# Kernel optimization log

Hardware: AMD Instinct MI355X
Metric: run time of the kernel (lower is better)

## Reference

```python
import jax, jax.numpy as jnp
import numpy as np

N = 50000
E = 800000
H = 128

def setup_inputs() -> dict:
    key = jax.random.key(0)
    ks = jax.random.split(key, 12)
    s = 1.0 / np.sqrt(H)
    inp = {
        "x": jax.random.normal(ks[0], (N, H), dtype=jnp.float32),
        "edge_index": jax.random.randint(ks[1], (2, E), 0, N, dtype=jnp.int64),
        "edge_attr": jax.random.normal(ks[2], (E, H), dtype=jnp.float32),
        # linear_edge: Linear(3H, H)
        "We": jax.random.uniform(ks[3], (3 * H, H), jnp.float32, -s, s),
        "be": jnp.zeros((H,), jnp.float32),
        # attention_layer.W: Linear(H, H)
        "Wg": jax.random.uniform(ks[4], (H, H), jnp.float32, -s, s),
        "bg": jnp.zeros((H,), jnp.float32),
        # attention_layer.a: Linear(2H, 1)
        "Wa": jax.random.uniform(ks[5], (2 * H, 1), jnp.float32, -s, s),
        "ba": jnp.zeros((1,), jnp.float32),
        # linear_out: Linear(H, H)
        "Wo": jax.random.uniform(ks[6], (H, H), jnp.float32, -s, s),
        "bo": jnp.zeros((H,), jnp.float32),
    }
    return inp


def reference(x, edge_index, edge_attr, We, be, Wg, bg, Wa, ba, Wo, bo):
    # PyG MessagePassing (flow=source_to_target): j = edge_index[0] (source),
    # i = edge_index[1] (target); aggregation scatters to edge_index[1].
    src = edge_index[0]
    dst = edge_index[1]

    # message: SiLU(Linear(cat[x_i, x_j, edge_attr]))  -- split We to avoid a [E,3H] concat
    m = jax.nn.silu(x[dst] @ We[:H] + x[src] @ We[H:2 * H] + edge_attr @ We[2 * H:] + be)  # [E,H]
    agg = jax.ops.segment_sum(m, dst, num_segments=N)  # [N,H] scatter-add aggregate

    # GraphAttentionLayer: row, col = edge_index -> row=edge_index[0], col=edge_index[1]
    h = agg @ Wg + bg  # [N,H]
    score = jax.nn.leaky_relu(h[src] @ Wa[:H] + h[dst] @ Wa[H:] + ba, negative_slope=0.2)  # [E,1]
    # softmax over the last dim of size 1 -> all ones (faithful to original); dropout off (eval)
    alpha = jax.nn.softmax(score, axis=-1)  # [E,1]
    attn_out = jax.ops.segment_sum(alpha * h[dst], src, num_segments=N)  # [N,H]

    return attn_out @ Wo + bo  # linear_out
```

## Files before the change

kernel.cpp:

```cpp
#include <hip/hip_runtime.h>

#define N_NODES 50000
#define N_EDGES 800000

typedef unsigned short u16;
typedef unsigned int u32;
typedef __attribute__((ext_vector_type(8))) short short8;
typedef __attribute__((ext_vector_type(4))) short s16x4;
typedef __attribute__((ext_vector_type(4))) float f32x4;

__device__ __forceinline__ u16 f2bf(float f) {
    union { float f; u32 u; } v; v.f = f;
    u32 r = v.u + 0x7FFFu + ((v.u >> 16) & 1u);
    return (u16)(r >> 16);
}

__device__ __forceinline__ float bf2f(u16 h) {
    union { u32 u; float f; } v; v.u = ((u32)h) << 16;
    return v.f;
}

__global__ __launch_bounds__(256) void compute_wc(const float* __restrict__ Wg,
                                                  const float* __restrict__ bg,
                                                  const float* __restrict__ Wo,
                                                  float* __restrict__ Wc,
                                                  float* __restrict__ bc) {
    int b = blockIdx.x;
    if (b < 8) {
        for (int i = 0; i < 8; ++i) {
            int o = b * 2048 + i * 256 + threadIdx.x;
            int k = o >> 7, n = o & 127;
            float s = 0.f;
            for (int j = 0; j < 128; ++j) s += Wg[k * 128 + j] * Wo[j * 128 + n];
            Wc[o] = s;
        }
    } else if (threadIdx.x < 128) {
        int n = threadIdx.x;
        float s = 0.f;
        for (int j = 0; j < 128; ++j) s += bg[j] * Wo[j * 128 + n];
        bc[n] = s;
    }
}

__global__ __launch_bounds__(256) void pack_all(const float* __restrict__ We,
                                                const float* __restrict__ Wc,
                                                const float* __restrict__ be,
                                                u16* __restrict__ PB1,
                                                u16* __restrict__ PB3,
                                                u16* __restrict__ PBc,
                                                float* __restrict__ b256) {
    int bid = blockIdx.x;
    int which = bid >> 3;
    const float* src;
    u16* dst;
    int tOff = 0;
    if (which == 0) { src = We; dst = PB1; }
    else if (which == 1) { src = We + 16384; dst = PB1; tOff = 8; }
    else if (which == 2) { src = We + 32768; dst = PB3; }
    else { src = Wc; dst = PBc; }
    int f = ((bid & 7) << 8) + threadIdx.x;
    int t = f >> 8, c = (f >> 6) & 3, lane = f & 63;
    int q = lane >> 4, n = lane & 15;
    const float* s = src + (size_t)(c * 32 + q * 8) * 128 + t * 16 + n;
    u16* dp = dst + ((((size_t)(t + tOff) * 4 + c) * 64 + lane) * 8);
#pragma unroll
    for (int j = 0; j < 8; ++j) dp[j] = f2bf(s[(size_t)j * 128]);
    if (bid == 0) b256[threadIdx.x] = (threadIdx.x < 128) ? be[threadIdx.x] : 0.f;
}

__global__ __launch_bounds__(256) void hist_kernel(const int* __restrict__ srcIdx,
                                                   const int* __restrict__ dstIdx,
                                                   int* __restrict__ degD,
                                                   int* __restrict__ degS) {
    int e = blockIdx.x * 256 + threadIdx.x;
    if (e >= N_EDGES) return;
    atomicAdd(&degD[dstIdx[e]], 1);
    atomicAdd(&degS[srcIdx[e]], 1);
}

__global__ __launch_bounds__(256) void scan_kernel(const int* __restrict__ degD,
                                                   const int* __restrict__ degS,
                                                   int* __restrict__ offD, int* __restrict__ curD,
                                                   int* __restrict__ offS, int* __restrict__ curS) {
    const int* deg = blockIdx.x ? degS : degD;
    int* off = blockIdx.x ? offS : offD;
    int* cur = blockIdx.x ? curS : curD;
    __shared__ int buf[256];
    const int CHUNK = 196;
    int tid = threadIdx.x;
    int s0 = tid * CHUNK, s1 = s0 + CHUNK;
    if (s1 > N_NODES) s1 = N_NODES;
    int s = 0;
    for (int i = s0; i < s1; ++i) s += deg[i];
    buf[tid] = s;
    __syncthreads();
    for (int o = 1; o < 256; o <<= 1) {
        int v = (tid >= o) ? buf[tid - o] : 0;
        __syncthreads();
        buf[tid] += v;
        __syncthreads();
    }
    int run = (tid > 0) ? buf[tid - 1] : 0;
    for (int i = s0; i < s1; ++i) {
        off[i] = run;
        cur[i] = run;
        run += deg[i];
    }
    if (tid == 255) off[N_NODES] = buf[255];
}

__global__ __launch_bounds__(256) void scatter_kernel(const int* __restrict__ srcIdx,
                                                      const int* __restrict__ dstIdx,
                                                      int* __restrict__ curD,
                                                      int* __restrict__ curS,
                                                      int* __restrict__ sd_ea,
                                                      int* __restrict__ sd_src,
                                                      int* __restrict__ ss_dst) {
    int e = blockIdx.x * 256 + threadIdx.x;
    if (e >= N_EDGES) return;
    int s = srcIdx[e], d = dstIdx[e];
    int p = atomicAdd(&curD[d], 1);
    sd_ea[p] = e;
    sd_src[p] = s;
    int p2 = atomicAdd(&curS[s], 1);
    ss_dst[p2] = d;
}

__global__ __launch_bounds__(256) void gemm_mfma(const void* __restrict__ Ap,
                                                 const u16* __restrict__ PB,
                                                 const float* __restrict__ bias,
                                                 const float* __restrict__ bias2,
                                                 const int* __restrict__ rowdeg,
                                                 void* __restrict__ outp,
                                                 int M, int Ctiles, int flags) {
    int tid = threadIdx.x;
    int wave = tid >> 6;
    int lane = tid & 63;
    int strip = blockIdx.x * 4 + wave;
    int row0 = strip * 16;
    if (row0 >= M) return;
    int q = lane >> 4, n = lane & 15;
    int C = Ctiles * 16;

    short8 a[4];
    if (flags & 2) {
        const u16* ap = (const u16*)Ap + (size_t)(row0 + n) * 128 + q * 8;
#pragma unroll
        for (int c = 0; c < 4; ++c) a[c] = *(const short8*)(ap + c * 32);
    } else {
        const float* ap = (const float*)Ap + (size_t)(row0 + n) * 128 + q * 8;
#pragma unroll
        for (int c = 0; c < 4; ++c) {
            f32x4 f0 = *(const f32x4*)(ap + c * 32);
            f32x4 f1 = *(const f32x4*)(ap + c * 32 + 4);
            short8 t;
#pragma unroll
            for (int j = 0; j < 4; ++j) {
                t[j] = (short)f2bf(f0[j]);
                t[4 + j] = (short)f2bf(f1[j]);
            }
            a[c] = t;
        }
    }

    float rb[4] = {0.f, 0.f, 0.f, 0.f};
    if (flags & 4) {
#pragma unroll
        for (int r = 0; r < 4; ++r) rb[r] = (float)rowdeg[row0 + q * 4 + r];
    }

    for (int t = 0; t < Ctiles; ++t) {
        f32x4 acc = {0.f, 0.f, 0.f, 0.f};
#pragma unroll
        for (int c = 0; c < 4; ++c) {
            short8 b = *(const short8*)(PB + (((size_t)t * 4 + c) * 64 + lane) * 8);
            acc = __builtin_amdgcn_mfma_f32_16x16x32_bf16(a[c], b, acc, 0, 0, 0);
        }
        int col = t * 16 + n;
        float bv = bias ? bias[col] : 0.f;
        float b2 = (flags & 4) ? bias2[col] : 0.f;
#pragma unroll
        for (int r = 0; r < 4; ++r) {
            int row = row0 + q * 4 + r;
            float v = acc[r] + bv + rb[r] * b2;
            if (flags & 1)
                ((u16*)outp)[(size_t)row * C + col] = f2bf(v);
            else
                ((float*)outp)[(size_t)row * C + col] = v;
        }
    }
}

__global__ __launch_bounds__(256) void agg_fused(const float* __restrict__ EA,
                                                 const u16* __restrict__ PB3,
                                                 const int* __restrict__ offD,
                                                 const int* __restrict__ sd_ea,
                                                 const int* __restrict__ sd_src,
                                                 const u16* __restrict__ T1,
                                                 u16* __restrict__ agg) {
    __shared__ u16 ldsT[4][16][132];
    int tid = threadIdx.x;
    int wave = tid >> 6;
    int lane = tid & 63;
    int node = blockIdx.x * 4 + wave;
    if (node >= N_NODES) return;
    int q = lane >> 4, n = lane & 15;
    int segS = offD[node], segE = offD[node + 1];

    float g1[8], rowAcc[8];
#pragma unroll
    for (int t = 0; t < 8; ++t) {
        g1[t] = bf2f(T1[(size_t)node * 256 + t * 16 + n]);
        rowAcc[t] = 0.f;
    }

    int rl = lane >> 2, cb = lane & 3;
    u16* myL = &ldsT[wave][0][0];

    for (int base = segS; base < segE; base += 16) {
        int er = base + n;
        if (er > segE - 1) er = segE - 1;
        const float* ap = EA + (size_t)sd_ea[er] * 128 + q * 8;
        short8 a[4];
#pragma unroll
        for (int c = 0; c < 4; ++c) {
            f32x4 f0 = *(const f32x4*)(ap + c * 32);
            f32x4 f1 = *(const f32x4*)(ap + c * 32 + 4);
            short8 t;
#pragma unroll
            for (int j = 0; j < 4; ++j) {
                t[j] = (short)f2bf(f0[j]);
                t[4 + j] = (short)f2bf(f1[j]);
            }
            a[c] = t;
        }

        int erL = base + rl;
        if (erL > segE - 1) erL = segE - 1;
        const u16* tb = T1 + (size_t)sd_src[erL] * 256 + 128;
        asm volatile("s_waitcnt lgkmcnt(0)" ::: "memory");
#pragma unroll
        for (int i = 0; i < 4; ++i) {
            short8 v = *(const short8*)(tb + (i * 4 + cb) * 8);
            s16x4 lo = __builtin_shufflevector(v, v, 0, 1, 2, 3);
            s16x4 hi = __builtin_shufflevector(v, v, 4, 5, 6, 7);
            *(s16x4*)(myL + rl * 132 + (i * 4 + cb) * 8) = lo;
            *(s16x4*)(myL + rl * 132 + (i * 4 + cb) * 8 + 4) = hi;
        }
        asm volatile("s_waitcnt lgkmcnt(0)" ::: "memory");

        bool val[4];
#pragma unroll
        for (int r = 0; r < 4; ++r) val[r] = (base + q * 4 + r) < segE;

#pragma unroll
        for (int t = 0; t < 8; ++t) {
            f32x4 acc = {0.f, 0.f, 0.f, 0.f};
#pragma unroll
            for (int c = 0; c < 4; ++c) {
                short8 b = *(const short8*)(PB3 + (((size_t)t * 4 + c) * 64 + lane) * 8);
                acc = __builtin_amdgcn_mfma_f32_16x16x32_bf16(a[c], b, acc, 0, 0, 0);
            }
#pragma unroll
            for (int r = 0; r < 4; ++r) {
                float v = acc[r] + g1[t] + bf2f(myL[(q * 4 + r) * 132 + t * 16 + n]);
                float m = v * __builtin_amdgcn_rcpf(1.f + __expf(-v));
                rowAcc[t] += val[r] ? m : 0.f;
            }
        }
    }
#pragma unroll
    for (int t = 0; t < 8; ++t) {
        float v = rowAcc[t];
        v += __shfl_xor(v, 16, 64);
        v += __shfl_xor(v, 32, 64);
        if (lane < 16) agg[(size_t)node * 128 + t * 16 + lane] = f2bf(v);
    }
}

__global__ __launch_bounds__(256) void attn_gather(const int* __restrict__ offS,
                                                   const int* __restrict__ ss_dst,
                                                   const u16* __restrict__ hsrc,
                                                   float* __restrict__ attn) {
    int tid = threadIdx.x;
    int wave = tid >> 6;
    int lane = tid & 63;
    int node = blockIdx.x * 4 + wave;
    if (node >= N_NODES) return;
    int e0 = offS[node], e1 = offS[node + 1];
    int half = lane >> 5;
    int l = lane & 31;
    float a0 = 0.f, a1 = 0.f, a2 = 0.f, a3 = 0.f;
    int e = e0 + half;
    for (; e + 6 < e1; e += 8) {
        int d0 = ss_dst[e], d1 = ss_dst[e + 2], d2 = ss_dst[e + 4], d3 = ss_dst[e + 6];
        uint2 h0 = *(const uint2*)(hsrc + (size_t)d0 * 128 + l * 4);
        uint2 h1 = *(const uint2*)(hsrc + (size_t)d1 * 128 + l * 4);
        uint2 h2 = *(const uint2*)(hsrc + (size_t)d2 * 128 + l * 4);
        uint2 h3 = *(const uint2*)(hsrc + (size_t)d3 * 128 + l * 4);
        a0 += bf2f((u16)(h0.x & 0xFFFFu)) + bf2f((u16)(h1.x & 0xFFFFu)) +
              bf2f((u16)(h2.x & 0xFFFFu)) + bf2f((u16)(h3.x & 0xFFFFu));
        a1 += bf2f((u16)(h0.x >> 16)) + bf2f((u16)(h1.x >> 16)) +
              bf2f((u16)(h2.x >> 16)) + bf2f((u16)(h3.x >> 16));
        a2 += bf2f((u16)(h0.y & 0xFFFFu)) + bf2f((u16)(h1.y & 0xFFFFu)) +
              bf2f((u16)(h2.y & 0xFFFFu)) + bf2f((u16)(h3.y & 0xFFFFu));
        a3 += bf2f((u16)(h0.y >> 16)) + bf2f((u16)(h1.y >> 16)) +
              bf2f((u16)(h2.y >> 16)) + bf2f((u16)(h3.y >> 16));
    }
    for (; e < e1; e += 2) {
        int d = ss_dst[e];
        uint2 hv = *(const uint2*)(hsrc + (size_t)d * 128 + l * 4);
        a0 += bf2f((u16)(hv.x & 0xFFFFu));
        a1 += bf2f((u16)(hv.x >> 16));
        a2 += bf2f((u16)(hv.y & 0xFFFFu));
        a3 += bf2f((u16)(hv.y >> 16));
    }
    a0 += __shfl_xor(a0, 32, 64);
    a1 += __shfl_xor(a1, 32, 64);
    a2 += __shfl_xor(a2, 32, 64);
    a3 += __shfl_xor(a3, 32, 64);
    if (half == 0) {
        f32x4 o;
        o[0] = a0; o[1] = a1; o[2] = a2; o[3] = a3;
        *(f32x4*)(attn + (size_t)node * 128 + l * 4) = o;
    }
}

extern "C" void kernel_launch(void* const* d_in, const int* in_sizes, int n_in,
                              void* d_out, int out_size, void* d_ws, size_t ws_size,
                              hipStream_t stream) {
    const float* x  = (const float*)d_in[0];
    const int* ei   = (const int*)d_in[1];
    const float* ea = (const float*)d_in[2];
    const float* We = (const float*)d_in[3];
    const float* be = (const float*)d_in[4];
    const float* Wg = (const float*)d_in[5];
    const float* bg = (const float*)d_in[6];
    const float* Wo = (const float*)d_in[9];
    const float* bo = (const float*)d_in[10];
    float* out = (float*)d_out;

    const int* srcIdx = ei;
    const int* dstIdx = ei + N_EDGES;

    char* ws = (char*)d_ws;
    u16*   PB1     = (u16*)(ws + 0);
    u16*   PB3     = (u16*)(ws + 65536);
    u16*   PBc     = (u16*)(ws + 98304);
    float* Wc      = (float*)(ws + 131072);
    float* bias256 = (float*)(ws + 196608);
    float* bc      = (float*)(ws + 197632);
    u16*   T1      = (u16*)(ws + 262144);
    float* attn    = (float*)(ws + 262144);
    u16*   agg     = (u16*)(ws + 25862144);
    int*   degD    = (int*)(ws + 51462144);
    int*   degS    = (int*)(ws + 51662144);
    int*   offD    = (int*)(ws + 51862144);
    int*   offS    = (int*)(ws + 52062160);
    int*   curD    = (int*)(ws + 52262176);
    int*   curS    = (int*)(ws + 52462176);
    int*   sd_ea   = (int*)(ws + 52662176);
    int*   sd_src  = (int*)(ws + 55862176);
    int*   ss_dst  = (int*)(ws + 59062176);

    hipMemsetAsync(degD, 0, 400000, stream);

    compute_wc<<<9, 256, 0, stream>>>(Wg, bg, Wo, Wc, bc);
    pack_all<<<32, 256, 0, stream>>>(We, Wc, be, PB1, PB3, PBc, bias256);

    hist_kernel<<<3125, 256, 0, stream>>>(srcIdx, dstIdx, degD, degS);
    scan_kernel<<<2, 256, 0, stream>>>(degD, degS, offD, curD, offS, curS);
    scatter_kernel<<<3125, 256, 0, stream>>>(srcIdx, dstIdx, curD, curS, sd_ea, sd_src, ss_dst);

    gemm_mfma<<<782, 256, 0, stream>>>(x, PB1, bias256, nullptr, nullptr, T1, N_NODES, 16, 1);

    agg_fused<<<12500, 256, 0, stream>>>(ea, PB3, offD, sd_ea, sd_src, T1, agg);

    attn_gather<<<12500, 256, 0, stream>>>(offS, ss_dst, agg, attn);

    gemm_mfma<<<782, 256, 0, stream>>>(attn, PBc, bo, bc, degS, out, N_NODES, 8, 4);

    (void)in_sizes; (void)n_in; (void)out_size; (void)ws_size;
}
```

Measured before the change: 1.102 ms.

## Fold source-node projection into edge MFMA and rebalance aggregation kernels

The edge kernel no longer gathers a precomputed x_src@We projection from T1 through LDS. It instead gathers bf16-cast x rows for the source node and runs a K=256 MFMA over the concatenated edge_attr and x_src against a combined packed weight. Each node's 128 output columns are now split across two waves, and edge id and source index are stored as one int2 to cut index loads. The attention gather now has a whole wave read 64 indices at once and broadcast them by shuffle, with each lane loading 2 bf16 values per edge. In exchange, the edge path does twice the MFMA work, and a separate cast kernel plus extra x-row gathers are added.

```diff
diff --git a/kernel.cpp b/kernel.cpp
--- a/kernel.cpp
+++ b/kernel.cpp
@@ -6,8 +6,8 @@
 typedef unsigned short u16;
 typedef unsigned int u32;
 typedef __attribute__((ext_vector_type(8))) short short8;
-typedef __attribute__((ext_vector_type(4))) short s16x4;
 typedef __attribute__((ext_vector_type(4))) float f32x4;
+typedef __attribute__((ext_vector_type(2))) float f32x2;
 
 __device__ __forceinline__ u16 f2bf(float f) {
     union { float f; u32 u; } v; v.f = f;
@@ -44,28 +44,35 @@
 
 __global__ __launch_bounds__(256) void pack_all(const float* __restrict__ We,
                                                 const float* __restrict__ Wc,
-                                                const float* __restrict__ be,
                                                 u16* __restrict__ PB1,
-                                                u16* __restrict__ PB3,
-                                                u16* __restrict__ PBc,
-                                                float* __restrict__ b256) {
+                                                u16* __restrict__ PBe,
+                                                u16* __restrict__ PBc) {
     int bid = blockIdx.x;
-    int which = bid >> 3;
-    const float* src;
-    u16* dst;
-    int tOff = 0;
-    if (which == 0) { src = We; dst = PB1; }
-    else if (which == 1) { src = We + 16384; dst = PB1; tOff = 8; }
-    else if (which == 2) { src = We + 32768; dst = PB3; }
-    else { src = Wc; dst = PBc; }
-    int f = ((bid & 7) << 8) + threadIdx.x;
-    int t = f >> 8, c = (f >> 6) & 3, lane = f & 63;
+    int job = bid >> 3;
+    int t = bid & 7;
+    const float* src; u16* dst; int slotBase, CH;
+    if (job == 0)      { src = We;         dst = PB1; slotBase = 0; CH = 4; }
+    else if (job == 1) { src = We + 32768; dst = PBe; slotBase = 0; CH = 8; }
+    else if (job == 2) { src = We + 16384; dst = PBe; slotBase = 4; CH = 8; }
+    else               { src = Wc;         dst = PBc; slotBase = 0; CH = 4; }
+    int c = threadIdx.x >> 6;
+    int lane = threadIdx.x & 63;
     int q = lane >> 4, n = lane & 15;
     const float* s = src + (size_t)(c * 32 + q * 8) * 128 + t * 16 + n;
-    u16* dp = dst + ((((size_t)(t + tOff) * 4 + c) * 64 + lane) * 8);
+    u16* dp = dst + (((size_t)(t * CH + slotBase + c) * 64 + lane) * 8);
 #pragma unroll
     for (int j = 0; j < 8; ++j) dp[j] = f2bf(s[(size_t)j * 128]);
-    if (bid == 0) b256[threadIdx.x] = (threadIdx.x < 128) ? be[threadIdx.x] : 0.f;
+}
+
+__global__ __launch_bounds__(256) void cast_bf16(const float* __restrict__ x,
+                                                 u16* __restrict__ X2) {
+    size_t i = (size_t)(blockIdx.x * 256 + threadIdx.x) * 8;
+    f32x4 v0 = *(const f32x4*)(x + i);
+    f32x4 v1 = *(const f32x4*)(x + i + 4);
+    short8 o;
+#pragma unroll
+    for (int j = 0; j < 4; ++j) { o[j] = (short)f2bf(v0[j]); o[4 + j] = (short)f2bf(v1[j]); }
+    *(short8*)(X2 + i) = o;
 }
 
 __global__ __launch_bounds__(256) void hist_kernel(const int* __restrict__ srcIdx,
@@ -113,15 +120,13 @@
                                                       const int* __restrict__ dstIdx,
                                                       int* __restrict__ curD,
                                                       int* __restrict__ curS,
-                                                      int* __restrict__ sd_ea,
-                                                      int* __restrict__ sd_src,
+                                                      int2* __restrict__ sdP,
                                                       int* __restrict__ ss_dst) {
     int e = blockIdx.x * 256 + threadIdx.x;
     if (e >= N_EDGES) return;
     int s = srcIdx[e], d = dstIdx[e];
     int p = atomicAdd(&curD[d], 1);
-    sd_ea[p] = e;
-    sd_src[p] = s;
+    sdP[p] = make_int2(e, s);
     int p2 = atomicAdd(&curS[s], 1);
     ss_dst[p2] = d;
 }
@@ -192,36 +197,36 @@
 }
 
 __global__ __launch_bounds__(256) void agg_fused(const float* __restrict__ EA,
-                                                 const u16* __restrict__ PB3,
+                                                 const u16* __restrict__ X2,
+                                                 const u16* __restrict__ PBe,
                                                  const int* __restrict__ offD,
-                                                 const int* __restrict__ sd_ea,
-                                                 const int* __restrict__ sd_src,
-                                                 const u16* __restrict__ T1,
+                                                 const int2* __restrict__ sdP,
+                                                 const u16* __restrict__ T1a,
                                                  u16* __restrict__ agg) {
-    __shared__ u16 ldsT[4][16][132];
     int tid = threadIdx.x;
     int wave = tid >> 6;
     int lane = tid & 63;
-    int node = blockIdx.x * 4 + wave;
+    int node = blockIdx.x * 2 + (wave >> 1);
     if (node >= N_NODES) return;
+    int cg = wave & 1;
     int q = lane >> 4, n = lane & 15;
     int segS = offD[node], segE = offD[node + 1];
-
-    float g1[8], rowAcc[8];
-#pragma unroll
-    for (int t = 0; t < 8; ++t) {
-        g1[t] = bf2f(T1[(size_t)node * 256 + t * 16 + n]);
+    const u16* pb = PBe + (size_t)cg * 16384;
+
+    float g1[4], rowAcc[4];
+#pragma unroll
+    for (int t = 0; t < 4; ++t) {
+        g1[t] = bf2f(T1a[(size_t)node * 128 + (cg * 4 + t) * 16 + n]);
         rowAcc[t] = 0.f;
     }
-
-    int rl = lane >> 2, cb = lane & 3;
-    u16* myL = &ldsT[wave][0][0];
 
     for (int base = segS; base < segE; base += 16) {
         int er = base + n;
         if (er > segE - 1) er = segE - 1;
-        const float* ap = EA + (size_t)sd_ea[er] * 128 + q * 8;
-        short8 a[4];
+        int2 es = sdP[er];
+        const float* ap = EA + (size_t)es.x * 128 + q * 8;
+        const u16* xp = X2 + (size_t)es.y * 128 + q * 8;
+        short8 a[8];
 #pragma unroll
         for (int c = 0; c < 4; ++c) {
             f32x4 f0 = *(const f32x4*)(ap + c * 32);
@@ -233,48 +238,34 @@
                 t[4 + j] = (short)f2bf(f1[j]);
             }
             a[c] = t;
-        }
-
-        int erL = base + rl;
-        if (erL > segE - 1) erL = segE - 1;
-        const u16* tb = T1 + (size_t)sd_src[erL] * 256 + 128;
-        asm volatile("s_waitcnt lgkmcnt(0)" ::: "memory");
-#pragma unroll
-        for (int i = 0; i < 4; ++i) {
-            short8 v = *(const short8*)(tb + (i * 4 + cb) * 8);
-            s16x4 lo = __builtin_shufflevector(v, v, 0, 1, 2, 3);
-            s16x4 hi = __builtin_shufflevector(v, v, 4, 5, 6, 7);
-            *(s16x4*)(myL + rl * 132 + (i * 4 + cb) * 8) = lo;
-            *(s16x4*)(myL + rl * 132 + (i * 4 + cb) * 8 + 4) = hi;
-        }
-        asm volatile("s_waitcnt lgkmcnt(0)" ::: "memory");
-
+            a[4 + c] = *(const short8*)(xp + c * 32);
+        }
         bool val[4];
 #pragma unroll
         for (int r = 0; r < 4; ++r) val[r] = (base + q * 4 + r) < segE;
 
 #pragma unroll
-        for (int t = 0; t < 8; ++t) {
+        for (int t = 0; t < 4; ++t) {
             f32x4 acc = {0.f, 0.f, 0.f, 0.f};
 #pragma unroll
-            for (int c = 0; c < 4; ++c) {
-                short8 b = *(const short8*)(PB3 + (((size_t)t * 4 + c) * 64 + lane) * 8);
+            for (int c = 0; c < 8; ++c) {
+                short8 b = *(const short8*)(pb + (((size_t)t * 8 + c) * 64 + lane) * 8);
                 acc = __builtin_amdgcn_mfma_f32_16x16x32_bf16(a[c], b, acc, 0, 0, 0);
             }
 #pragma unroll
             for (int r = 0; r < 4; ++r) {
-                float v = acc[r] + g1[t] + bf2f(myL[(q * 4 + r) * 132 + t * 16 + n]);
+                float v = acc[r] + g1[t];
                 float m = v * __builtin_amdgcn_rcpf(1.f + __expf(-v));
                 rowAcc[t] += val[r] ? m : 0.f;
             }
         }
     }
 #pragma unroll
-    for (int t = 0; t < 8; ++t) {
+    for (int t = 0; t < 4; ++t) {
         float v = rowAcc[t];
         v += __shfl_xor(v, 16, 64);
         v += __shfl_xor(v, 32, 64);
-        if (lane < 16) agg[(size_t)node * 128 + t * 16 + lane] = f2bf(v);
+        if (lane < 16) agg[(size_t)node * 128 + (cg * 4 + t) * 16 + lane] = f2bf(v);
     }
 }
 
@@ -288,42 +279,38 @@
     int node = blockIdx.x * 4 + wave;
     if (node >= N_NODES) return;
     int e0 = offS[node], e1 = offS[node + 1];
-    int half = lane >> 5;
-    int l = lane & 31;
-    float a0 = 0.f, a1 = 0.f, a2 = 0.f, a3 = 0.f;
-    int e = e0 + half;
-    for (; e + 6 < e1; e += 8) {
-        int d0 = ss_dst[e], d1 = ss_dst[e + 2], d2 = ss_dst[e + 4], d3 = ss_dst[e + 6];
-        uint2 h0 = *(const uint2*)(hsrc + (size_t)d0 * 128 + l * 4);
-        uint2 h1 = *(const uint2*)(hsrc + (size_t)d1 * 128 + l * 4);
-        uint2 h2 = *(const uint2*)(hsrc + (size_t)d2 * 128 + l * 4);
-        uint2 h3 = *(const uint2*)(hsrc + (size_t)d3 * 128 + l * 4);
-        a0 += bf2f((u16)(h0.x & 0xFFFFu)) + bf2f((u16)(h1.x & 0xFFFFu)) +
-              bf2f((u16)(h2.x & 0xFFFFu)) + bf2f((u16)(h3.x & 0xFFFFu));
-        a1 += bf2f((u16)(h0.x >> 16)) + bf2f((u16)(h1.x >> 16)) +
-              bf2f((u16)(h2.x >> 16)) + bf2f((u16)(h3.x >> 16));
-        a2 += bf2f((u16)(h0.y & 0xFFFFu)) + bf2f((u16)(h1.y & 0xFFFFu)) +
-              bf2f((u16)(h2.y & 0xFFFFu)) + bf2f((u16)(h3.y & 0xFFFFu));
-        a3 += bf2f((u16)(h0.y >> 16)) + bf2f((u16)(h1.y >> 16)) +
-              bf2f((u16)(h2.y >> 16)) + bf2f((u16)(h3.y >> 16));
-    }
-    for (; e < e1; e += 2) {
-        int d = ss_dst[e];
-        uint2 hv = *(const uint2*)(hsrc + (size_t)d * 128 + l * 4);
-        a0 += bf2f((u16)(hv.x & 0xFFFFu));
-        a1 += bf2f((u16)(hv.x >> 16));
-        a2 += bf2f((u16)(hv.y & 0xFFFFu));
-        a3 += bf2f((u16)(hv.y >> 16));
-    }
-    a0 += __shfl_xor(a0, 32, 64);
-    a1 += __shfl_xor(a1, 32, 64);
-    a2 += __shfl_xor(a2, 32, 64);
-    a3 += __shfl_xor(a3, 32, 64);
-    if (half == 0) {
-        f32x4 o;
-        o[0] = a0; o[1] = a1; o[2] = a2; o[3] = a3;
-        *(f32x4*)(attn + (size_t)node * 128 + l * 4) = o;
-    }
+    float a0 = 0.f, a1 = 0.f;
+    for (int base = e0; base < e1; base += 64) {
+        int m = e1 - base;
+        if (m > 64) m = 64;
+        int ii = lane < m ? lane : m - 1;
+        int myIdx = ss_dst[base + ii];
+        int j = 0;
+        for (; j + 4 <= m; j += 4) {
+            int d0 = __shfl(myIdx, j, 64);
+            int d1 = __shfl(myIdx, j + 1, 64);
+            int d2 = __shfl(myIdx, j + 2, 64);
+            int d3 = __shfl(myIdx, j + 3, 64);
+            u32 h0 = *(const u32*)(hsrc + (size_t)d0 * 128 + lane * 2);
+            u32 h1 = *(const u32*)(hsrc + (size_t)d1 * 128 + lane * 2);
+            u32 h2 = *(const u32*)(hsrc + (size_t)d2 * 128 + lane * 2);
+            u32 h3 = *(const u32*)(hsrc + (size_t)d3 * 128 + lane * 2);
+            a0 += bf2f((u16)(h0 & 0xFFFFu)) + bf2f((u16)(h1 & 0xFFFFu)) +
+                  bf2f((u16)(h2 & 0xFFFFu)) + bf2f((u16)(h3 & 0xFFFFu));
+            a1 += bf2f((u16)(h0 >> 16)) + bf2f((u16)(h1 >> 16)) +
+                  bf2f((u16)(h2 >> 16)) + bf2f((u16)(h3 >> 16));
+        }
+        for (; j < m; ++j) {
+            int d = __shfl(myIdx, j, 64);
+            u32 h = *(const u32*)(hsrc + (size_t)d * 128 + lane * 2);
+            a0 += bf2f((u16)(h & 0xFFFFu));
+            a1 += bf2f((u16)(h >> 16));
+        }
+    }
+    f32x2 o;
+    o[0] = a0;
+    o[1] = a1;
+    *(f32x2*)(attn + (size_t)node * 128 + lane * 2) = o;
 }
 
 extern "C" void kernel_launch(void* const* d_in, const int* in_sizes, int n_in,
@@ -344,37 +331,38 @@
     const int* dstIdx = ei + N_EDGES;
 
     char* ws = (char*)d_ws;
-    u16*   PB1     = (u16*)(ws + 0);
-    u16*   PB3     = (u16*)(ws + 65536);
-    u16*   PBc     = (u16*)(ws + 98304);
-    float* Wc      = (float*)(ws + 131072);
-    float* bias256 = (float*)(ws + 196608);
-    float* bc      = (float*)(ws + 197632);
-    u16*   T1      = (u16*)(ws + 262144);
-    float* attn    = (float*)(ws + 262144);
-    u16*   agg     = (u16*)(ws + 25862144);
-    int*   degD    = (int*)(ws + 51462144);
-    int*   degS    = (int*)(ws + 51662144);
-    int*   offD    = (int*)(ws + 51862144);
-    int*   offS    = (int*)(ws + 52062160);
-    int*   curD    = (int*)(ws + 52262176);
-    int*   curS    = (int*)(ws + 52462176);
-    int*   sd_ea   = (int*)(ws + 52662176);
-    int*   sd_src  = (int*)(ws + 55862176);
-    int*   ss_dst  = (int*)(ws + 59062176);
+    u16*   PB1    = (u16*)(ws + 0);
+    u16*   PBe    = (u16*)(ws + 32768);
+    u16*   PBc    = (u16*)(ws + 98304);
+    float* Wc     = (float*)(ws + 131072);
+    float* bc     = (float*)(ws + 196608);
+    u16*   T1a    = (u16*)(ws + 262144);
+    u16*   X2     = (u16*)(ws + 13062144);
+    float* attn   = (float*)(ws + 262144);
+    u16*   agg    = (u16*)(ws + 25862144);
+    int*   degD   = (int*)(ws + 38662144);
+    int*   degS   = (int*)(ws + 38862144);
+    int*   offD   = (int*)(ws + 39062144);
+    int*   offS   = (int*)(ws + 39262160);
+    int*   curD   = (int*)(ws + 39462176);
+    int*   curS   = (int*)(ws + 39662176);
+    int2*  sdP    = (int2*)(ws + 39862176);
+    int*   ss_dst = (int*)(ws + 46262176);
 
     hipMemsetAsync(degD, 0, 400000, stream);
 
     compute_wc<<<9, 256, 0, stream>>>(Wg, bg, Wo, Wc, bc);
-    pack_all<<<32, 256, 0, stream>>>(We, Wc, be, PB1, PB3, PBc, bias256);
+    pack_all<<<32, 256, 0, stream>>>(We, Wc, PB1, PBe, PBc);
 
     hist_kernel<<<3125, 256, 0, stream>>>(srcIdx, dstIdx, degD, degS);
     scan_kernel<<<2, 256, 0, stream>>>(degD, degS, offD, curD, offS, curS);
-    scatter_kernel<<<3125, 256, 0, stream>>>(srcIdx, dstIdx, curD, curS, sd_ea, sd_src, ss_dst);
-
-    gemm_mfma<<<782, 256, 0, stream>>>(x, PB1, bias256, nullptr, nullptr, T1, N_NODES, 16, 1);
-
-    agg_fused<<<12500, 256, 0, stream>>>(ea, PB3, offD, sd_ea, sd_src, T1, agg);
+    scatter_kernel<<<3125, 256, 0, stream>>>(srcIdx, dstIdx, curD, curS, sdP, ss_dst);
+
+    cast_bf16<<<3125, 256, 0, stream>>>(x, X2);
+
+    gemm_mfma<<<782, 256, 0, stream>>>(x, PB1, be, nullptr, nullptr, T1a, N_NODES, 8, 1);
+
+    agg_fused<<<25000, 256, 0, stream>>>(ea, X2, PBe, offD, sdP, T1a, agg);
 
     attn_gather<<<12500, 256, 0, stream>>>(offS, ss_dst, agg, attn);
 
```

After: 1.253 ms. 13.7% more time.
